# Optimization experiments

Measured on AMD Instinct MI355X. Metric: run time of the kernel, lower is better.

The kernel has to match this reference:

```python
import jax, jax.numpy as jnp
import numpy as np

B, N, H, F, E, G, O = 4, 1024, 128, 128, 16, 128, 128


def setup_inputs() -> dict:
    key = jax.random.key(0)
    ks = jax.random.split(key, 16)
    hidden = jax.random.normal(ks[0], (B, N, H), dtype=jnp.float32)
    n_features = jax.random.normal(ks[1], (B, N, F), dtype=jnp.float32)
    e_features = jax.random.normal(ks[2], (B, N, N, E), dtype=jnp.float32)
    g_features = jax.random.normal(ks[3], (B, G), dtype=jnp.float32)
    # random 0/1 adjacency with self-loops
    adj = (jax.random.uniform(ks[4], (B, N, N)) < 0.5).astype(jnp.float32)
    adj = jnp.maximum(adj, jnp.eye(N, dtype=jnp.float32)[None])
    Din = F + H  # concat([n_features, hidden])
    s = 1.0 / np.sqrt(Din)
    W_m = jax.random.normal(ks[5], (Din, O), dtype=jnp.float32) * s
    b_m = jnp.zeros((O,), dtype=jnp.float32)
    W_skip = jax.random.normal(ks[6], (Din, O), dtype=jnp.float32) * s
    b_skip = jnp.zeros((O,), dtype=jnp.float32)
    w_a1 = jax.random.normal(ks[7], (Din, 1), dtype=jnp.float32) * s
    b_a1 = jnp.zeros((1,), dtype=jnp.float32)
    w_a2 = jax.random.normal(ks[8], (Din, 1), dtype=jnp.float32) * s
    b_a2 = jnp.zeros((1,), dtype=jnp.float32)
    w_ae = jax.random.normal(ks[9], (E, 1), dtype=jnp.float32) / np.sqrt(E)
    b_ae = jnp.zeros((1,), dtype=jnp.float32)
    w_ag = jax.random.normal(ks[10], (G, 1), dtype=jnp.float32) / np.sqrt(G)
    b_ag = jnp.zeros((1,), dtype=jnp.float32)
    return {
        'hidden': hidden, 'n_features': n_features, 'e_features': e_features,
        'g_features': g_features, 'adj': adj,
        'W_m': W_m, 'b_m': b_m, 'W_skip': W_skip, 'b_skip': b_skip,
        'w_a1': w_a1, 'b_a1': b_a1, 'w_a2': w_a2, 'b_a2': b_a2,
        'w_ae': w_ae, 'b_ae': b_ae, 'w_ag': w_ag, 'b_ag': b_ag,
    }


def reference(hidden, n_features, e_features, g_features, adj,
              W_m, b_m, W_skip, b_skip, w_a1, b_a1, w_a2, b_a2,
              w_ae, b_ae, w_ag, b_ag):
    features = jnp.concatenate([n_features, hidden], axis=-1)  # [B,N,F+H]
    bias_mat = (adj - 1.0) * 1e9  # [B,N,N]
    values = features @ W_m + b_m                              # [B,N,O]
    att_1 = features @ w_a1 + b_a1                             # [B,N,1]
    att_2 = features @ w_a2 + b_a2                             # [B,N,1]
    att_e = jnp.squeeze(e_features @ w_ae + b_ae, axis=-1)     # [B,N,N]
    att_g = g_features @ w_ag + b_ag                           # [B,1]
    logits = att_1 + jnp.transpose(att_2, (0, 2, 1)) + att_e + att_g[:, :, None]
    coefs = jax.nn.softmax(jax.nn.leaky_relu(logits) + bias_mat, axis=-1)
    ret = jnp.matmul(coefs, values)                            # [B,N,O]
    ret = ret + (features @ W_skip + b_skip)                   # residual
    return ret
```

## Files before the change

### kernel.cpp

```cpp
#include <hip/hip_runtime.h>
#include <hip/hip_bf16.h>

#define B_ 4
#define N_ 1024
#define H_ 128
#define F_ 128
#define E_ 16
#define G_ 128
#define O_ 128
#define DIN 256

__global__ __launch_bounds__(256) void k_att(
    const float* __restrict__ nf, const float* __restrict__ hid,
    const float* __restrict__ wa1, const float* __restrict__ ba1,
    const float* __restrict__ wa2, const float* __restrict__ ba2,
    const float* __restrict__ gf, const float* __restrict__ wag,
    const float* __restrict__ bag,
    float* __restrict__ att1, float* __restrict__ att2, float* __restrict__ attg) {
  const int t = threadIdx.x;
  const int w = t >> 6;
  const int lane = t & 63;

  if (blockIdx.x == (N_ * B_) / 4) {
    if (w < B_) {
      const int b = w;
      float2 g2 = *reinterpret_cast<const float2*>(gf + b * G_ + lane * 2);
      float2 wg = *reinterpret_cast<const float2*>(wag + lane * 2);
      float p = g2.x * wg.x + g2.y * wg.y;
      #pragma unroll
      for (int off = 32; off; off >>= 1) p += __shfl_xor(p, off);
      if (lane == 0) attg[b] = p + bag[0];
    }
    return;
  }

  const int g = blockIdx.x * 4 + w;
  const int c = lane * 4;
  const float* src = (c < F_) ? (nf + (size_t)g * F_ + c)
                              : (hid + (size_t)g * H_ + (c - F_));
  float4 f = *reinterpret_cast<const float4*>(src);
  float4 w1 = *reinterpret_cast<const float4*>(wa1 + c);
  float4 w2 = *reinterpret_cast<const float4*>(wa2 + c);
  float p1 = f.x * w1.x + f.y * w1.y + f.z * w1.z + f.w * w1.w;
  float p2 = f.x * w2.x + f.y * w2.y + f.z * w2.z + f.w * w2.w;
  #pragma unroll
  for (int off = 32; off; off >>= 1) {
    p1 += __shfl_xor(p1, off);
    p2 += __shfl_xor(p2, off);
  }
  if (lane == 0) {
    att1[g] = p1 + ba1[0];
    att2[g] = p2 + ba2[0];
  }
}

__global__ __launch_bounds__(256) void k_gemm(
    const float* __restrict__ nf, const float* __restrict__ hid,
    const float* __restrict__ Wm, const float* __restrict__ bm,
    const float* __restrict__ Wsk, const float* __restrict__ bsk,
    float* __restrict__ values, float* __restrict__ out) {
  __shared__ float4 feat[16][64];
  const int t = threadIdx.x;
  const int g0 = blockIdx.x * 16;

  #pragma unroll
  for (int q = 0; q < 4; ++q) {
    int flat = q * 256 + t;
    int r = flat >> 6;
    int c4 = flat & 63;
    int g = g0 + r;
    int c = c4 * 4;
    const float* src = (c < F_) ? (nf + (size_t)g * F_ + c)
                                : (hid + (size_t)g * H_ + (c - F_));
    feat[r][c4] = *reinterpret_cast<const float4*>(src);
  }
  __syncthreads();

  const int col = t & 127;
  const float* W = (t < 128) ? Wm : Wsk;
  const float bias = (t < 128) ? bm[col] : bsk[col];

  float acc[16];
  #pragma unroll
  for (int r = 0; r < 16; ++r) acc[r] = 0.f;

  for (int k4 = 0; k4 < 64; ++k4) {
    float w0 = W[(k4 * 4 + 0) * O_ + col];
    float w1 = W[(k4 * 4 + 1) * O_ + col];
    float w2 = W[(k4 * 4 + 2) * O_ + col];
    float w3 = W[(k4 * 4 + 3) * O_ + col];
    #pragma unroll
    for (int r = 0; r < 16; ++r) {
      float4 f = feat[r][k4];
      acc[r] = fmaf(f.x, w0, acc[r]);
      acc[r] = fmaf(f.y, w1, acc[r]);
      acc[r] = fmaf(f.z, w2, acc[r]);
      acc[r] = fmaf(f.w, w3, acc[r]);
    }
  }

  #pragma unroll
  for (int r = 0; r < 16; ++r) {
    size_t idx = (size_t)(g0 + r) * O_ + col;
    if (t < 128) values[idx] = acc[r] + bias;
    else         out[idx]    = acc[r] + bias;
  }
}

__global__ __launch_bounds__(512) void k_main(
    const float* __restrict__ ef, const float* __restrict__ adj,
    const float* __restrict__ wae, const float* __restrict__ bae,
    const float* __restrict__ att1, const float* __restrict__ att2,
    const float* __restrict__ attg,
    const float* __restrict__ values, float* __restrict__ out) {
  __shared__ float att2_s[N_];
  __shared__ float p_s[8][N_];

  const int t = threadIdx.x;
  const int w = t >> 6;
  const int lane = t & 63;
  const int b = blockIdx.x >> 7;
  const int tile = blockIdx.x & 127;
  const int i0 = tile * 8;
  const int i = i0 + w;

  att2_s[t]       = att2[b * N_ + t];
  att2_s[t + 512] = att2[b * N_ + t + 512];
  __syncthreads();

  const float base = att1[b * N_ + i] + attg[b] + bae[0];
  const float4 we = *reinterpret_cast<const float4*>(wae + (lane & 3) * 4);
  const float4* erow =
      reinterpret_cast<const float4*>(ef + ((size_t)(b * N_ + i) * N_) * E_);
  const float* arow = adj + (size_t)(b * N_ + i) * N_;

  float mmax = -3.0e38f;
  for (int k = 0; k < 64; ++k) {
    float4 e = erow[k * 64 + lane];
    float part = e.x * we.x + e.y * we.y + e.z * we.z + e.w * we.w;
    part += __shfl_xor(part, 1);
    part += __shfl_xor(part, 2);
    int j = k * 16 + (lane >> 2);
    float l = base + att2_s[j] + part;
    l = (l >= 0.f) ? l : 0.01f * l;
    l += (arow[j] - 1.0f) * 1e9f;
    mmax = fmaxf(mmax, l);
    if ((lane & 3) == 0) p_s[w][j] = l;
  }
  #pragma unroll
  for (int off = 32; off; off >>= 1) mmax = fmaxf(mmax, __shfl_xor(mmax, off));

  float s = 0.f;
  #pragma unroll 4
  for (int q = 0; q < 16; ++q) {
    int j = q * 64 + lane;
    float p = __expf(p_s[w][j] - mmax);
    p_s[w][j] = p;
    s += p;
  }
  #pragma unroll
  for (int off = 32; off; off >>= 1) s += __shfl_xor(s, off);
  const float rs = 1.0f / s;

  const int jo = lane >> 5;
  const int o4 = (lane & 31) * 4;
  const float4* vb = reinterpret_cast<const float4*>(values + (size_t)b * N_ * O_);
  float4 acc = make_float4(0.f, 0.f, 0.f, 0.f);
  #pragma unroll 4
  for (int j = 0; j < N_; j += 2) {
    float pv = p_s[w][j + jo];
    float4 v = vb[(size_t)(j + jo) * 32 + (lane & 31)];
    acc.x = fmaf(pv, v.x, acc.x);
    acc.y = fmaf(pv, v.y, acc.y);
    acc.z = fmaf(pv, v.z, acc.z);
    acc.w = fmaf(pv, v.w, acc.w);
  }
  acc.x += __shfl_xor(acc.x, 32);
  acc.y += __shfl_xor(acc.y, 32);
  acc.z += __shfl_xor(acc.z, 32);
  acc.w += __shfl_xor(acc.w, 32);

  if (jo == 0) {
    size_t oidx = ((size_t)(b * N_ + i) * O_) + o4;
    float4 cur = *reinterpret_cast<const float4*>(out + oidx);
    cur.x += acc.x * rs;
    cur.y += acc.y * rs;
    cur.z += acc.z * rs;
    cur.w += acc.w * rs;
    *reinterpret_cast<float4*>(out + oidx) = cur;
  }
}

extern "C" void kernel_launch(void* const* d_in, const int* in_sizes, int n_in,
                              void* d_out, int out_size, void* d_ws, size_t ws_size,
                              hipStream_t stream) {
  const float* hidden = (const float*)d_in[0];
  const float* nf     = (const float*)d_in[1];
  const float* ef     = (const float*)d_in[2];
  const float* gf     = (const float*)d_in[3];
  const float* adj    = (const float*)d_in[4];
  const float* Wm     = (const float*)d_in[5];
  const float* bm     = (const float*)d_in[6];
  const float* Wsk    = (const float*)d_in[7];
  const float* bsk    = (const float*)d_in[8];
  const float* wa1    = (const float*)d_in[9];
  const float* ba1    = (const float*)d_in[10];
  const float* wa2    = (const float*)d_in[11];
  const float* ba2    = (const float*)d_in[12];
  const float* wae    = (const float*)d_in[13];
  const float* bae    = (const float*)d_in[14];
  const float* wag    = (const float*)d_in[15];
  const float* bag    = (const float*)d_in[16];

  float* out = (float*)d_out;
  float* ws = (float*)d_ws;
  float* values = ws;
  float* att1v  = ws + 524288;
  float* att2v  = ws + 528384;
  float* attgv  = ws + 532480;

  hipLaunchKernelGGL(k_att, dim3(N_ * B_ / 4 + 1), dim3(256), 0, stream,
                     nf, hidden, wa1, ba1, wa2, ba2, gf, wag, bag,
                     att1v, att2v, attgv);
  hipLaunchKernelGGL(k_gemm, dim3(B_ * N_ / 16), dim3(256), 0, stream,
                     nf, hidden, Wm, bm, Wsk, bsk, values, out);
  hipLaunchKernelGGL(k_main, dim3(B_ * N_ / 8), dim3(512), 0, stream,
                     ef, adj, wae, bae, att1v, att2v, attgv, values, out);
}
```

Measured before the change: 505.3 us.

## Share values loads across rows in attention matmul and batch edge-feature loads

In the main kernel, each wave now handles a 128-column slice of j for all 8 rows, not the full row for one row. Each values load is reused across 8 rows, with a cross-wave reduction through shared memory at the end. Edge-feature loads are batched 8 at a time to raise memory-level parallelism, and the logits/softmax pass now uses vectorized adj and shared-memory reads. The GEMM tile is halved to 8 rows to double the block count. The cost is more registers (8 float4 accumulators) and extra block-wide syncs.

```diff
diff --git a/kernel.cpp b/kernel.cpp
--- a/kernel.cpp
+++ b/kernel.cpp
@@ -59,12 +59,12 @@
     const float* __restrict__ Wm, const float* __restrict__ bm,
     const float* __restrict__ Wsk, const float* __restrict__ bsk,
     float* __restrict__ values, float* __restrict__ out) {
-  __shared__ float4 feat[16][64];
+  __shared__ float4 feat[8][64];
   const int t = threadIdx.x;
-  const int g0 = blockIdx.x * 16;
-
-  #pragma unroll
-  for (int q = 0; q < 4; ++q) {
+  const int g0 = blockIdx.x * 8;
+
+  #pragma unroll
+  for (int q = 0; q < 2; ++q) {
     int flat = q * 256 + t;
     int r = flat >> 6;
     int c4 = flat & 63;
@@ -80,17 +80,18 @@
   const float* W = (t < 128) ? Wm : Wsk;
   const float bias = (t < 128) ? bm[col] : bsk[col];
 
-  float acc[16];
-  #pragma unroll
-  for (int r = 0; r < 16; ++r) acc[r] = 0.f;
-
+  float acc[8];
+  #pragma unroll
+  for (int r = 0; r < 8; ++r) acc[r] = 0.f;
+
+  #pragma unroll 2
   for (int k4 = 0; k4 < 64; ++k4) {
     float w0 = W[(k4 * 4 + 0) * O_ + col];
     float w1 = W[(k4 * 4 + 1) * O_ + col];
     float w2 = W[(k4 * 4 + 2) * O_ + col];
     float w3 = W[(k4 * 4 + 3) * O_ + col];
     #pragma unroll
-    for (int r = 0; r < 16; ++r) {
+    for (int r = 0; r < 8; ++r) {
       float4 f = feat[r][k4];
       acc[r] = fmaf(f.x, w0, acc[r]);
       acc[r] = fmaf(f.y, w1, acc[r]);
@@ -100,7 +101,7 @@
   }
 
   #pragma unroll
-  for (int r = 0; r < 16; ++r) {
+  for (int r = 0; r < 8; ++r) {
     size_t idx = (size_t)(g0 + r) * O_ + col;
     if (t < 128) values[idx] = acc[r] + bias;
     else         out[idx]    = acc[r] + bias;
@@ -128,65 +129,118 @@
   att2_s[t + 512] = att2[b * N_ + t + 512];
   __syncthreads();
 
-  const float base = att1[b * N_ + i] + attg[b] + bae[0];
   const float4 we = *reinterpret_cast<const float4*>(wae + (lane & 3) * 4);
   const float4* erow =
       reinterpret_cast<const float4*>(ef + ((size_t)(b * N_ + i) * N_) * E_);
-  const float* arow = adj + (size_t)(b * N_ + i) * N_;
-
-  float mmax = -3.0e38f;
-  for (int k = 0; k < 64; ++k) {
-    float4 e = erow[k * 64 + lane];
-    float part = e.x * we.x + e.y * we.y + e.z * we.z + e.w * we.w;
-    part += __shfl_xor(part, 1);
-    part += __shfl_xor(part, 2);
-    int j = k * 16 + (lane >> 2);
-    float l = base + att2_s[j] + part;
-    l = (l >= 0.f) ? l : 0.01f * l;
-    l += (arow[j] - 1.0f) * 1e9f;
-    mmax = fmaxf(mmax, l);
-    if ((lane & 3) == 0) p_s[w][j] = l;
-  }
-  #pragma unroll
-  for (int off = 32; off; off >>= 1) mmax = fmaxf(mmax, __shfl_xor(mmax, off));
+  for (int kk = 0; kk < 64; kk += 8) {
+    float4 e[8];
+    #pragma unroll
+    for (int u = 0; u < 8; ++u) e[u] = erow[(kk + u) * 64 + lane];
+    #pragma unroll
+    for (int u = 0; u < 8; ++u) {
+      float part = e[u].x * we.x + e[u].y * we.y + e[u].z * we.z + e[u].w * we.w;
+      part += __shfl_xor(part, 1);
+      part += __shfl_xor(part, 2);
+      if ((lane & 3) == 0) p_s[w][(kk + u) * 16 + (lane >> 2)] = part;
+    }
+  }
+
+  const float base = att1[b * N_ + i] + attg[b] + bae[0];
+  const float4* adj4 =
+      reinterpret_cast<const float4*>(adj + (size_t)(b * N_ + i) * N_);
+  float4 la[4];
+  float vmax = -3.0e38f;
+  #pragma unroll
+  for (int q = 0; q < 4; ++q) {
+    int j4 = q * 64 + lane;
+    float4 p4 = *reinterpret_cast<const float4*>(&p_s[w][j4 * 4]);
+    float4 a4 = adj4[j4];
+    float4 t2 = *reinterpret_cast<const float4*>(&att2_s[j4 * 4]);
+    float4 l;
+    l.x = base + t2.x + p4.x; l.x = (l.x >= 0.f) ? l.x : 0.01f * l.x; l.x += (a4.x - 1.f) * 1e9f;
+    l.y = base + t2.y + p4.y; l.y = (l.y >= 0.f) ? l.y : 0.01f * l.y; l.y += (a4.y - 1.f) * 1e9f;
+    l.z = base + t2.z + p4.z; l.z = (l.z >= 0.f) ? l.z : 0.01f * l.z; l.z += (a4.z - 1.f) * 1e9f;
+    l.w = base + t2.w + p4.w; l.w = (l.w >= 0.f) ? l.w : 0.01f * l.w; l.w += (a4.w - 1.f) * 1e9f;
+    la[q] = l;
+    vmax = fmaxf(vmax, fmaxf(fmaxf(l.x, l.y), fmaxf(l.z, l.w)));
+  }
+  #pragma unroll
+  for (int off = 32; off; off >>= 1) vmax = fmaxf(vmax, __shfl_xor(vmax, off));
 
   float s = 0.f;
-  #pragma unroll 4
-  for (int q = 0; q < 16; ++q) {
-    int j = q * 64 + lane;
-    float p = __expf(p_s[w][j] - mmax);
-    p_s[w][j] = p;
-    s += p;
+  #pragma unroll
+  for (int q = 0; q < 4; ++q) {
+    la[q].x = __expf(la[q].x - vmax);
+    la[q].y = __expf(la[q].y - vmax);
+    la[q].z = __expf(la[q].z - vmax);
+    la[q].w = __expf(la[q].w - vmax);
+    s += la[q].x + la[q].y + la[q].z + la[q].w;
   }
   #pragma unroll
   for (int off = 32; off; off >>= 1) s += __shfl_xor(s, off);
   const float rs = 1.0f / s;
+  #pragma unroll
+  for (int q = 0; q < 4; ++q) {
+    float4 p;
+    p.x = la[q].x * rs; p.y = la[q].y * rs; p.z = la[q].z * rs; p.w = la[q].w * rs;
+    *reinterpret_cast<float4*>(&p_s[w][(q * 64 + lane) * 4]) = p;
+  }
+  __syncthreads();
 
   const int jo = lane >> 5;
-  const int o4 = (lane & 31) * 4;
+  const int l31 = lane & 31;
   const float4* vb = reinterpret_cast<const float4*>(values + (size_t)b * N_ * O_);
-  float4 acc = make_float4(0.f, 0.f, 0.f, 0.f);
+  float4 acc[8];
+  #pragma unroll
+  for (int r = 0; r < 8; ++r) acc[r] = make_float4(0.f, 0.f, 0.f, 0.f);
+
+  const int jbase = w * 128;
   #pragma unroll 4
-  for (int j = 0; j < N_; j += 2) {
-    float pv = p_s[w][j + jo];
-    float4 v = vb[(size_t)(j + jo) * 32 + (lane & 31)];
-    acc.x = fmaf(pv, v.x, acc.x);
-    acc.y = fmaf(pv, v.y, acc.y);
-    acc.z = fmaf(pv, v.z, acc.z);
-    acc.w = fmaf(pv, v.w, acc.w);
-  }
-  acc.x += __shfl_xor(acc.x, 32);
-  acc.y += __shfl_xor(acc.y, 32);
-  acc.z += __shfl_xor(acc.z, 32);
-  acc.w += __shfl_xor(acc.w, 32);
-
+  for (int it = 0; it < 64; ++it) {
+    int jj = jbase + it * 2 + jo;
+    float4 v = vb[(size_t)jj * 32 + l31];
+    #pragma unroll
+    for (int r = 0; r < 8; ++r) {
+      float pv = p_s[r][jj];
+      acc[r].x = fmaf(pv, v.x, acc[r].x);
+      acc[r].y = fmaf(pv, v.y, acc[r].y);
+      acc[r].z = fmaf(pv, v.z, acc[r].z);
+      acc[r].w = fmaf(pv, v.w, acc[r].w);
+    }
+  }
+  #pragma unroll
+  for (int r = 0; r < 8; ++r) {
+    acc[r].x += __shfl_xor(acc[r].x, 32);
+    acc[r].y += __shfl_xor(acc[r].y, 32);
+    acc[r].z += __shfl_xor(acc[r].z, 32);
+    acc[r].w += __shfl_xor(acc[r].w, 32);
+  }
+  __syncthreads();
+
+  float* part = &p_s[0][0];
   if (jo == 0) {
-    size_t oidx = ((size_t)(b * N_ + i) * O_) + o4;
+    #pragma unroll
+    for (int r = 0; r < 8; ++r)
+      *reinterpret_cast<float4*>(part + (w * 8 + r) * 128 + l31 * 4) = acc[r];
+  }
+  __syncthreads();
+
+  float4 sum = make_float4(0.f, 0.f, 0.f, 0.f);
+  #pragma unroll
+  for (int u = 0; u < 4; ++u) {
+    int wsrc = jo * 4 + u;
+    float4 p = *reinterpret_cast<const float4*>(part + (wsrc * 8 + w) * 128 + l31 * 4);
+    sum.x += p.x; sum.y += p.y; sum.z += p.z; sum.w += p.w;
+  }
+  sum.x += __shfl_xor(sum.x, 32);
+  sum.y += __shfl_xor(sum.y, 32);
+  sum.z += __shfl_xor(sum.z, 32);
+  sum.w += __shfl_xor(sum.w, 32);
+
+  if (jo == 0) {
+    size_t oidx = ((size_t)(b * N_ + i) * O_) + l31 * 4;
     float4 cur = *reinterpret_cast<const float4*>(out + oidx);
-    cur.x += acc.x * rs;
-    cur.y += acc.y * rs;
-    cur.z += acc.z * rs;
-    cur.w += acc.w * rs;
+    cur.x += sum.x; cur.y += sum.y; cur.z += sum.z; cur.w += sum.w;
     *reinterpret_cast<float4*>(out + oidx) = cur;
   }
 }
@@ -222,7 +276,7 @@
   hipLaunchKernelGGL(k_att, dim3(N_ * B_ / 4 + 1), dim3(256), 0, stream,
                      nf, hidden, wa1, ba1, wa2, ba2, gf, wag, bag,
                      att1v, att2v, attgv);
-  hipLaunchKernelGGL(k_gemm, dim3(B_ * N_ / 16), dim3(256), 0, stream,
+  hipLaunchKernelGGL(k_gemm, dim3(B_ * N_ / 8), dim3(256), 0, stream,
                      nf, hidden, Wm, bm, Wsk, bsk, values, out);
   hipLaunchKernelGGL(k_main, dim3(B_ * N_ / 8), dim3(512), 0, stream,
                      ef, adj, wae, bae, att1v, att2v, attgv, values, out);
```

After: 428.7 us. -15.2%, faster.
